# Kernel tuning notes

Hardware: AMD Instinct MI355X
Metric: run time of the kernel (lower is better)

## Reference

```python
import jax, jax.numpy as jnp
import numpy as np
from jax import lax

BETA = 0.95
THRESHOLD = 1.0
B, T, D_IN, D_OUT = 128, 512, 512, 512


def setup_inputs() -> dict:
    key = jax.random.key(0)
    k1, k2, k3 = jax.random.split(key, 3)
    x_seq = jax.random.normal(k1, (B, T, D_IN), dtype=jnp.float32)
    W = jax.random.normal(k2, (D_OUT, D_IN), dtype=jnp.float32) * (1.0 / np.sqrt(D_IN))
    b = jax.random.normal(k3, (D_OUT,), dtype=jnp.float32) * 0.01
    return {"x_seq": x_seq, "W": W, "b": b}


def reference(x_seq, W, b):
    # Batch the linear across all timesteps: [B,T,D_in] @ [D_out,D_in]^T -> [B,T,D_out]
    currents = jnp.einsum('bti,oi->bto', x_seq, W) + b

    def step(mem, cur):  # mem: [B, D_out], cur: [B, D_out]
        mem = BETA * mem + cur
        spk = (mem > THRESHOLD).astype(mem.dtype)
        return mem - spk * THRESHOLD, spk

    mem0 = jnp.zeros((x_seq.shape[0], W.shape[0]), dtype=x_seq.dtype)
    _, spikes_tbd = lax.scan(step, mem0, jnp.swapaxes(currents, 0, 1))  # [T,B,D]
    spikes = jnp.swapaxes(spikes_tbd, 0, 1)  # [B,T,D]
    return spikes, spikes.sum()
```

## Files before the change

### kernel.cpp

```cpp
#include <hip/hip_runtime.h>
#include <hip/hip_bf16.h>

#define M_TOT 65536
#define K_DIM 512
#define N_DIM 512
#define T_STEPS 512
#define BETA 0.95f

#define BM 128
#define BN 128
#define BK 64

typedef __attribute__((ext_vector_type(8))) short bf16x8;
typedef __attribute__((ext_vector_type(8))) unsigned short u16x8;
typedef __attribute__((ext_vector_type(4))) float f32x4;

#define X_ELEMS ((size_t)M_TOT * K_DIM)
#define W_ELEMS ((size_t)N_DIM * K_DIM)
#define WS_NEEDED ((X_ELEMS + W_ELEMS) * 2)

static __device__ __forceinline__ unsigned short f2bf(float f) {
    __hip_bfloat16 h = __float2bfloat16(f);
    return __builtin_bit_cast(unsigned short, h);
}

__global__ __launch_bounds__(256) void convert_bf16(
    const float* __restrict__ X, const float* __restrict__ W,
    unsigned short* __restrict__ Xb, unsigned short* __restrict__ Wb,
    float* __restrict__ sum_out)
{
    const size_t gid = (size_t)blockIdx.x * 256 + threadIdx.x;
    if (gid == 0) *sum_out = 0.0f;
    const size_t NXT = X_ELEMS / 8;
    if (gid < NXT) {
        const float4 v0 = *(const float4*)(X + gid * 8);
        const float4 v1 = *(const float4*)(X + gid * 8 + 4);
        u16x8 o;
        o[0] = f2bf(v0.x); o[1] = f2bf(v0.y); o[2] = f2bf(v0.z); o[3] = f2bf(v0.w);
        o[4] = f2bf(v1.x); o[5] = f2bf(v1.y); o[6] = f2bf(v1.z); o[7] = f2bf(v1.w);
        *(u16x8*)(Xb + gid * 8) = o;
    } else {
        const size_t g2 = gid - NXT;
        const float4 v0 = *(const float4*)(W + g2 * 8);
        const float4 v1 = *(const float4*)(W + g2 * 8 + 4);
        u16x8 o;
        o[0] = f2bf(v0.x); o[1] = f2bf(v0.y); o[2] = f2bf(v0.z); o[3] = f2bf(v0.w);
        o[4] = f2bf(v1.x); o[5] = f2bf(v1.y); o[6] = f2bf(v1.z); o[7] = f2bf(v1.w);
        *(u16x8*)(Wb + g2 * 8) = o;
    }
}

__global__ __launch_bounds__(256) void gemm_fast(
    const unsigned short* __restrict__ Xb,
    const unsigned short* __restrict__ Wb,
    const float* __restrict__ bias,
    float* __restrict__ C)
{
    __shared__ alignas(16) unsigned short Xs[BM][BK];
    __shared__ alignas(16) unsigned short Ws[BN][BK];

    const int lin  = blockIdx.x;
    const int swz  = (lin & 7) * 256 + (lin >> 3);
    const int mtile = swz >> 2;
    const int ntile = swz & 3;

    const int tid  = threadIdx.x;
    const int lane = tid & 63;
    const int wave = tid >> 6;
    const int wr = wave >> 1;
    const int wc = wave & 1;

    const int row0 = mtile * BM;
    const int col0 = ntile * BN;

    f32x4 acc[4][4] = {};

    const int srow = lane >> 3;
    const int scb  = (lane & 7) ^ (srow & 7);
    const unsigned short* xsrc[4];
    const unsigned short* wsrc[4];
    #pragma unroll
    for (int j = 0; j < 4; ++j) {
        const int ra = row0 + wave * 32 + j * 8 + srow;
        const int rb = col0 + wave * 32 + j * 8 + srow;
        xsrc[j] = Xb + (size_t)ra * K_DIM + scb * 8;
        wsrc[j] = Wb + (size_t)rb * K_DIM + scb * 8;
    }

    const int frow = lane & 15;
    const int cblk = lane >> 4;

    #pragma unroll
    for (int t = 0; t < 8; ++t) {
        if (t) __syncthreads();
        #pragma unroll
        for (int j = 0; j < 4; ++j) {
            __builtin_amdgcn_global_load_lds(
                (const __attribute__((address_space(1))) unsigned int*)(const void*)(xsrc[j] + t * BK),
                (__attribute__((address_space(3))) unsigned int*)(void*)(&Xs[wave * 32 + j * 8][0]),
                16, 0, 0);
            __builtin_amdgcn_global_load_lds(
                (const __attribute__((address_space(1))) unsigned int*)(const void*)(wsrc[j] + t * BK),
                (__attribute__((address_space(3))) unsigned int*)(void*)(&Ws[wave * 32 + j * 8][0]),
                16, 0, 0);
        }
        __syncthreads();

        #pragma unroll
        for (int kh = 0; kh < 2; ++kh) {
            bf16x8 afr[4], bfr[4];
            #pragma unroll
            for (int m = 0; m < 4; ++m) {
                int row = wr * 64 + m * 16 + frow;
                int c = (kh * 4 + cblk) ^ (row & 7);
                afr[m] = *(const bf16x8*)(&Xs[row][c * 8]);
            }
            #pragma unroll
            for (int n = 0; n < 4; ++n) {
                int row = wc * 64 + n * 16 + frow;
                int c = (kh * 4 + cblk) ^ (row & 7);
                bfr[n] = *(const bf16x8*)(&Ws[row][c * 8]);
            }
            #pragma unroll
            for (int m = 0; m < 4; ++m)
                #pragma unroll
                for (int n = 0; n < 4; ++n)
                    acc[m][n] = __builtin_amdgcn_mfma_f32_16x16x32_bf16(
                        afr[m], bfr[n], acc[m][n], 0, 0, 0);
        }
    }

    const int crow_base = (lane >> 4) * 4;
    const int ccol = lane & 15;
    #pragma unroll
    for (int n = 0; n < 4; ++n) {
        int col = col0 + wc * 64 + n * 16 + ccol;
        float bv = bias[col];
        #pragma unroll
        for (int m = 0; m < 4; ++m) {
            int rowb = row0 + wr * 64 + m * 16 + crow_base;
            #pragma unroll
            for (int r = 0; r < 4; ++r) {
                C[(size_t)(rowb + r) * N_DIM + col] = acc[m][n][r] + bv;
            }
        }
    }
}

static __device__ __forceinline__ void stage_tiles(
    unsigned short (*__restrict__ Xs)[BK], unsigned short (*__restrict__ Ws)[BK],
    const float4* xr, const float4* wv, int sr0, int skg)
{
    #pragma unroll
    for (int i = 0; i < 8; ++i) {
        int r   = sr0 + i * 16;
        int kgs = skg ^ ((r & 7) << 3);
        ushort4 xb, wb;
        xb.x = f2bf(xr[i].x); xb.y = f2bf(xr[i].y); xb.z = f2bf(xr[i].z); xb.w = f2bf(xr[i].w);
        wb.x = f2bf(wv[i].x); wb.y = f2bf(wv[i].y); wb.z = f2bf(wv[i].z); wb.w = f2bf(wv[i].w);
        *(ushort4*)(&Xs[r][kgs]) = xb;
        *(ushort4*)(&Ws[r][kgs]) = wb;
    }
}

__global__ __launch_bounds__(256, 2) void gemm_slow(
    const float* __restrict__ X, const float* __restrict__ W,
    const float* __restrict__ bias, float* __restrict__ C,
    float* __restrict__ sum_out)
{
    __shared__ unsigned short Xs[2][BM][BK];
    __shared__ unsigned short Ws[2][BN][BK];

    const int lin  = blockIdx.x;
    const int swz  = (lin & 7) * 256 + (lin >> 3);
    const int mtile = swz >> 2;
    const int ntile = swz & 3;

    const int tid  = threadIdx.x;
    const int lane = tid & 63;
    const int wave = tid >> 6;
    const int wr = wave >> 1;
    const int wc = wave & 1;

    if (lin == 0 && tid == 0) *sum_out = 0.0f;

    const int row0 = mtile * BM;
    const int col0 = ntile * BN;

    f32x4 acc[4][4] = {};

    const int sr0 = tid >> 4;
    const int skg = (tid & 15) << 2;
    const float* xbase = X + (size_t)row0 * K_DIM + skg;
    const float* wbase = W + (size_t)col0 * K_DIM + skg;

    float4 xr[8], wv[8];
    #pragma unroll
    for (int i = 0; i < 8; ++i) {
        int r = sr0 + i * 16;
        xr[i] = *(const float4*)(xbase + (size_t)r * K_DIM);
        wv[i] = *(const float4*)(wbase + (size_t)r * K_DIM);
    }
    stage_tiles(Xs[0], Ws[0], xr, wv, sr0, skg);

    const int frow = lane & 15;
    const int cblk = lane >> 4;

    for (int t = 0; t < 8; ++t) {
        __syncthreads();
        if (t < 7) {
            const int k0n = (t + 1) * BK;
            #pragma unroll
            for (int i = 0; i < 8; ++i) {
                int r = sr0 + i * 16;
                xr[i] = *(const float4*)(xbase + (size_t)r * K_DIM + k0n);
                wv[i] = *(const float4*)(wbase + (size_t)r * K_DIM + k0n);
            }
        }
        unsigned short (*Xb)[BK] = Xs[t & 1];
        unsigned short (*Wb)[BK] = Ws[t & 1];
        #pragma unroll
        for (int kh = 0; kh < 2; ++kh) {
            bf16x8 afr[4], bfr[4];
            #pragma unroll
            for (int m = 0; m < 4; ++m) {
                int row = wr * 64 + m * 16 + frow;
                int c = (kh * 4 + cblk) ^ (row & 7);
                afr[m] = *(const bf16x8*)(&Xb[row][c * 8]);
            }
            #pragma unroll
            for (int n = 0; n < 4; ++n) {
                int row = wc * 64 + n * 16 + frow;
                int c = (kh * 4 + cblk) ^ (row & 7);
                bfr[n] = *(const bf16x8*)(&Wb[row][c * 8]);
            }
            #pragma unroll
            for (int m = 0; m < 4; ++m)
                #pragma unroll
                for (int n = 0; n < 4; ++n)
                    acc[m][n] = __builtin_amdgcn_mfma_f32_16x16x32_bf16(
                        afr[m], bfr[n], acc[m][n], 0, 0, 0);
        }
        if (t < 7)
            stage_tiles(Xs[(t + 1) & 1], Ws[(t + 1) & 1], xr, wv, sr0, skg);
    }

    const int crow_base = (lane >> 4) * 4;
    const int ccol = lane & 15;
    #pragma unroll
    for (int n = 0; n < 4; ++n) {
        int col = col0 + wc * 64 + n * 16 + ccol;
        float bv = bias[col];
        #pragma unroll
        for (int m = 0; m < 4; ++m) {
            int rowb = row0 + wr * 64 + m * 16 + crow_base;
            #pragma unroll
            for (int r = 0; r < 4; ++r) {
                C[(size_t)(rowb + r) * N_DIM + col] = acc[m][n][r] + bv;
            }
        }
    }
}

__global__ __launch_bounds__(256) void lif_scan(
    float* __restrict__ C,
    float* __restrict__ sum_out)
{
    const int idx = blockIdx.x * 256 + threadIdx.x;
    float* p = C + (size_t)(idx >> 9) * (T_STEPS * N_DIM) + (idx & 511);

    float mem = 0.0f;
    int count = 0;
    float a[32], b[32];

    #pragma unroll
    for (int j = 0; j < 32; ++j)
        a[j] = p[(size_t)j * N_DIM];

    for (int t = 0; t < T_STEPS; t += 64) {
        #pragma unroll
        for (int j = 0; j < 32; ++j)
            b[j] = p[(size_t)(t + 32 + j) * N_DIM];
        #pragma unroll
        for (int j = 0; j < 32; ++j) {
            mem = BETA * mem + a[j];
            float spk = (mem > 1.0f) ? 1.0f : 0.0f;
            mem -= spk;
            __builtin_nontemporal_store(spk, p + (size_t)(t + j) * N_DIM);
            count += (int)spk;
        }
        if (t + 64 < T_STEPS) {
            #pragma unroll
            for (int j = 0; j < 32; ++j)
                a[j] = p[(size_t)(t + 64 + j) * N_DIM];
        }
        #pragma unroll
        for (int j = 0; j < 32; ++j) {
            mem = BETA * mem + b[j];
            float spk = (mem > 1.0f) ? 1.0f : 0.0f;
            mem -= spk;
            __builtin_nontemporal_store(spk, p + (size_t)(t + 32 + j) * N_DIM);
            count += (int)spk;
        }
    }

    #pragma unroll
    for (int off = 32; off > 0; off >>= 1)
        count += __shfl_down(count, off);
    __shared__ int wsum[4];
    if ((threadIdx.x & 63) == 0) wsum[threadIdx.x >> 6] = count;
    __syncthreads();
    if (threadIdx.x == 0) {
        int tot = wsum[0] + wsum[1] + wsum[2] + wsum[3];
        atomicAdd(sum_out, (float)tot);
    }
}

extern "C" void kernel_launch(void* const* d_in, const int* in_sizes, int n_in,
                              void* d_out, int out_size, void* d_ws, size_t ws_size,
                              hipStream_t stream) {
    const float* X    = (const float*)d_in[0];
    const float* W    = (const float*)d_in[1];
    const float* bias = (const float*)d_in[2];
    float* out = (float*)d_out;
    float* sum_slot = out + (size_t)M_TOT * N_DIM;

    if (ws_size >= WS_NEEDED) {
        unsigned short* Xb = (unsigned short*)d_ws;
        unsigned short* Wb = Xb + X_ELEMS;
        const int nconv = (int)((X_ELEMS / 8 + W_ELEMS / 8) / 256);
        convert_bf16<<<nconv, 256, 0, stream>>>(X, W, Xb, Wb, sum_slot);
        gemm_fast<<<(M_TOT / BM) * (N_DIM / BN), 256, 0, stream>>>(Xb, Wb, bias, out);
    } else {
        gemm_slow<<<(M_TOT / BM) * (N_DIM / BN), 256, 0, stream>>>(X, W, bias, out, sum_slot);
    }
    lif_scan<<<M_TOT / 256, 256, 0, stream>>>(out, sum_slot);
}
```

Baseline: 315.5 us.

## Store GEMM output as bf16 in workspace and double-buffer LDS loads

The GEMM now writes bias-added currents as bf16 into a workspace buffer instead of fp32 into the output. The scan reads these bf16 values and writes fp32 spikes to the output, which halves the intermediate write and read traffic. The fast GEMM also gains double-buffered global_load_lds prefetch, so the next K tile loads while the current one is computed. Rounding currents to bf16 can flip spikes near the threshold and change the recurrence, and the workspace requirement grows.

```diff
diff --git a/kernel.cpp b/kernel.cpp
--- a/kernel.cpp
+++ b/kernel.cpp
@@ -17,11 +17,14 @@
 
 #define X_ELEMS ((size_t)M_TOT * K_DIM)
 #define W_ELEMS ((size_t)N_DIM * K_DIM)
-#define WS_NEEDED ((X_ELEMS + W_ELEMS) * 2)
+#define WS_NEEDED ((X_ELEMS + W_ELEMS + X_ELEMS) * 2)
 
 static __device__ __forceinline__ unsigned short f2bf(float f) {
     __hip_bfloat16 h = __float2bfloat16(f);
     return __builtin_bit_cast(unsigned short, h);
+}
+static __device__ __forceinline__ float bf2f(unsigned short u) {
+    return __builtin_bit_cast(float, (unsigned int)u << 16);
 }
 
 __global__ __launch_bounds__(256) void convert_bf16(
@@ -54,10 +57,10 @@
     const unsigned short* __restrict__ Xb,
     const unsigned short* __restrict__ Wb,
     const float* __restrict__ bias,
-    float* __restrict__ C)
-{
-    __shared__ alignas(16) unsigned short Xs[BM][BK];
-    __shared__ alignas(16) unsigned short Ws[BN][BK];
+    unsigned short* __restrict__ Cb)
+{
+    __shared__ alignas(16) unsigned short Xs[2][BM][BK];
+    __shared__ alignas(16) unsigned short Ws[2][BN][BK];
 
     const int lin  = blockIdx.x;
     const int swz  = (lin & 7) * 256 + (lin >> 3);
@@ -91,20 +94,35 @@
     const int cblk = lane >> 4;
 
     #pragma unroll
+    for (int j = 0; j < 4; ++j) {
+        __builtin_amdgcn_global_load_lds(
+            (const __attribute__((address_space(1))) unsigned int*)(const void*)(xsrc[j]),
+            (__attribute__((address_space(3))) unsigned int*)(void*)(&Xs[0][wave * 32 + j * 8][0]),
+            16, 0, 0);
+        __builtin_amdgcn_global_load_lds(
+            (const __attribute__((address_space(1))) unsigned int*)(const void*)(wsrc[j]),
+            (__attribute__((address_space(3))) unsigned int*)(void*)(&Ws[0][wave * 32 + j * 8][0]),
+            16, 0, 0);
+    }
+
+    #pragma unroll
     for (int t = 0; t < 8; ++t) {
-        if (t) __syncthreads();
-        #pragma unroll
-        for (int j = 0; j < 4; ++j) {
-            __builtin_amdgcn_global_load_lds(
-                (const __attribute__((address_space(1))) unsigned int*)(const void*)(xsrc[j] + t * BK),
-                (__attribute__((address_space(3))) unsigned int*)(void*)(&Xs[wave * 32 + j * 8][0]),
-                16, 0, 0);
-            __builtin_amdgcn_global_load_lds(
-                (const __attribute__((address_space(1))) unsigned int*)(const void*)(wsrc[j] + t * BK),
-                (__attribute__((address_space(3))) unsigned int*)(void*)(&Ws[wave * 32 + j * 8][0]),
-                16, 0, 0);
-        }
+        const int cur = t & 1;
         __syncthreads();
+
+        if (t < 7) {
+            #pragma unroll
+            for (int j = 0; j < 4; ++j) {
+                __builtin_amdgcn_global_load_lds(
+                    (const __attribute__((address_space(1))) unsigned int*)(const void*)(xsrc[j] + (t + 1) * BK),
+                    (__attribute__((address_space(3))) unsigned int*)(void*)(&Xs[cur ^ 1][wave * 32 + j * 8][0]),
+                    16, 0, 0);
+                __builtin_amdgcn_global_load_lds(
+                    (const __attribute__((address_space(1))) unsigned int*)(const void*)(wsrc[j] + (t + 1) * BK),
+                    (__attribute__((address_space(3))) unsigned int*)(void*)(&Ws[cur ^ 1][wave * 32 + j * 8][0]),
+                    16, 0, 0);
+            }
+        }
 
         #pragma unroll
         for (int kh = 0; kh < 2; ++kh) {
@@ -113,13 +131,13 @@
             for (int m = 0; m < 4; ++m) {
                 int row = wr * 64 + m * 16 + frow;
                 int c = (kh * 4 + cblk) ^ (row & 7);
-                afr[m] = *(const bf16x8*)(&Xs[row][c * 8]);
+                afr[m] = *(const bf16x8*)(&Xs[cur][row][c * 8]);
             }
             #pragma unroll
             for (int n = 0; n < 4; ++n) {
                 int row = wc * 64 + n * 16 + frow;
                 int c = (kh * 4 + cblk) ^ (row & 7);
-                bfr[n] = *(const bf16x8*)(&Ws[row][c * 8]);
+                bfr[n] = *(const bf16x8*)(&Ws[cur][row][c * 8]);
             }
             #pragma unroll
             for (int m = 0; m < 4; ++m)
@@ -141,9 +159,66 @@
             int rowb = row0 + wr * 64 + m * 16 + crow_base;
             #pragma unroll
             for (int r = 0; r < 4; ++r) {
-                C[(size_t)(rowb + r) * N_DIM + col] = acc[m][n][r] + bv;
-            }
-        }
+                Cb[(size_t)(rowb + r) * N_DIM + col] = f2bf(acc[m][n][r] + bv);
+            }
+        }
+    }
+}
+
+__global__ __launch_bounds__(256) void lif_scan(
+    const unsigned short* __restrict__ Cb,
+    float* __restrict__ S,
+    float* __restrict__ sum_out)
+{
+    const int idx = blockIdx.x * 256 + threadIdx.x;
+    const size_t base = (size_t)(idx >> 9) * (T_STEPS * N_DIM) + (idx & 511);
+    const unsigned short* p = Cb + base;
+    float* q = S + base;
+
+    float mem = 0.0f;
+    int count = 0;
+    float a[32], b[32];
+
+    #pragma unroll
+    for (int j = 0; j < 32; ++j)
+        a[j] = bf2f(p[(size_t)j * N_DIM]);
+
+    for (int t = 0; t < T_STEPS; t += 64) {
+        #pragma unroll
+        for (int j = 0; j < 32; ++j)
+            b[j] = bf2f(p[(size_t)(t + 32 + j) * N_DIM]);
+        #pragma unroll
+        for (int j = 0; j < 32; ++j) {
+            mem = BETA * mem + a[j];
+            float spk = (mem > 1.0f) ? 1.0f : 0.0f;
+            mem -= spk;
+            __builtin_nontemporal_store(spk, q + (size_t)(t + j) * N_DIM);
+            count += (int)spk;
+        }
+        if (t + 64 < T_STEPS) {
+            #pragma unroll
+            for (int j = 0; j < 32; ++j)
+                a[j] = bf2f(p[(size_t)(t + 64 + j) * N_DIM]);
+        }
+        #pragma unroll
+        for (int j = 0; j < 32; ++j) {
+            mem = BETA * mem + b[j];
+            float spk = (mem > 1.0f) ? 1.0f : 0.0f;
+            mem -= spk;
+            __builtin_nontemporal_store(spk, q + (size_t)(t + 32 + j) * N_DIM);
+            count += (int)spk;
+        }
+    }
+
+    #pragma unroll
+    for (int off = 32; off > 0; off >>= 1)
+        count += __shfl_down(count, off);
+    __shared__ int wsum[4];
+    if ((threadIdx.x & 63) == 0) wsum[threadIdx.x >> 6] = count;
+    __syncthreads();
+    if (threadIdx.x == 0) {
+        int tot = wsum[0] + wsum[1] + wsum[2] + wsum[3];
+        atomicAdd(sum_out, (float)tot);
     }
 }
 
@@ -217,8 +292,8 @@
                 wv[i] = *(const float4*)(wbase + (size_t)r * K_DIM + k0n);
             }
         }
-        unsigned short (*Xb)[BK] = Xs[t & 1];
-        unsigned short (*Wb)[BK] = Ws[t & 1];
+        unsigned short (*Xbuf)[BK] = Xs[t & 1];
+        unsigned short (*Wbuf)[BK] = Ws[t & 1];
         #pragma unroll
         for (int kh = 0; kh < 2; ++kh) {
             bf16x8 afr[4], bfr[4];
@@ -226,13 +301,13 @@
             for (int m = 0; m < 4; ++m) {
                 int row = wr * 64 + m * 16 + frow;
                 int c = (kh * 4 + cblk) ^ (row & 7);
-                afr[m] = *(const bf16x8*)(&Xb[row][c * 8]);
+                afr[m] = *(const bf16x8*)(&Xbuf[row][c * 8]);
             }
             #pragma unroll
             for (int n = 0; n < 4; ++n) {
                 int row = wc * 64 + n * 16 + frow;
                 int c = (kh * 4 + cblk) ^ (row & 7);
-                bfr[n] = *(const bf16x8*)(&Wb[row][c * 8]);
+                bfr[n] = *(const bf16x8*)(&Wbuf[row][c * 8]);
             }
             #pragma unroll
             for (int m = 0; m < 4; ++m)
@@ -262,58 +337,33 @@
     }
 }
 
-__global__ __launch_bounds__(256) void lif_scan(
-    float* __restrict__ C,
-    float* __restrict__ sum_out)
+__global__ __launch_bounds__(256) void lif_scan_f32(
+    float* __restrict__ C, float* __restrict__ sum_out)
 {
     const int idx = blockIdx.x * 256 + threadIdx.x;
     float* p = C + (size_t)(idx >> 9) * (T_STEPS * N_DIM) + (idx & 511);
-
     float mem = 0.0f;
     int count = 0;
-    float a[32], b[32];
-
-    #pragma unroll
-    for (int j = 0; j < 32; ++j)
-        a[j] = p[(size_t)j * N_DIM];
-
-    for (int t = 0; t < T_STEPS; t += 64) {
-        #pragma unroll
-        for (int j = 0; j < 32; ++j)
-            b[j] = p[(size_t)(t + 32 + j) * N_DIM];
-        #pragma unroll
-        for (int j = 0; j < 32; ++j) {
-            mem = BETA * mem + a[j];
+    for (int t = 0; t < T_STEPS; t += 8) {
+        float cur[8];
+        #pragma unroll
+        for (int j = 0; j < 8; ++j) cur[j] = p[(size_t)(t + j) * N_DIM];
+        #pragma unroll
+        for (int j = 0; j < 8; ++j) {
+            mem = BETA * mem + cur[j];
             float spk = (mem > 1.0f) ? 1.0f : 0.0f;
             mem -= spk;
-            __builtin_nontemporal_store(spk, p + (size_t)(t + j) * N_DIM);
+            p[(size_t)(t + j) * N_DIM] = spk;
             count += (int)spk;
         }
-        if (t + 64 < T_STEPS) {
-            #pragma unroll
-            for (int j = 0; j < 32; ++j)
-                a[j] = p[(size_t)(t + 64 + j) * N_DIM];
-        }
-        #pragma unroll
-        for (int j = 0; j < 32; ++j) {
-            mem = BETA * mem + b[j];
-            float spk = (mem > 1.0f) ? 1.0f : 0.0f;
-            mem -= spk;
-            __builtin_nontemporal_store(spk, p + (size_t)(t + 32 + j) * N_DIM);
-            count += (int)spk;
-        }
-    }
-
-    #pragma unroll
-    for (int off = 32; off > 0; off >>= 1)
-        count += __shfl_down(count, off);
+    }
+    #pragma unroll
+    for (int off = 32; off > 0; off >>= 1) count += __shfl_down(count, off);
     __shared__ int wsum[4];
     if ((threadIdx.x & 63) == 0) wsum[threadIdx.x >> 6] = count;
     __syncthreads();
-    if (threadIdx.x == 0) {
-        int tot = wsum[0] + wsum[1] + wsum[2] + wsum[3];
-        atomicAdd(sum_out, (float)tot);
-    }
+    if (threadIdx.x == 0)
+        atomicAdd(sum_out, (float)(wsum[0] + wsum[1] + wsum[2] + wsum[3]));
 }
 
 extern "C" void kernel_launch(void* const* d_in, const int* in_sizes, int n_in,
@@ -328,11 +378,13 @@
     if (ws_size >= WS_NEEDED) {
         unsigned short* Xb = (unsigned short*)d_ws;
         unsigned short* Wb = Xb + X_ELEMS;
+        unsigned short* Cb = Wb + W_ELEMS;
         const int nconv = (int)((X_ELEMS / 8 + W_ELEMS / 8) / 256);
         convert_bf16<<<nconv, 256, 0, stream>>>(X, W, Xb, Wb, sum_slot);
-        gemm_fast<<<(M_TOT / BM) * (N_DIM / BN), 256, 0, stream>>>(Xb, Wb, bias, out);
+        gemm_fast<<<(M_TOT / BM) * (N_DIM / BN), 256, 0, stream>>>(Xb, Wb, bias, Cb);
+        lif_scan<<<M_TOT / 256, 256, 0, stream>>>(Cb, out, sum_slot);
     } else {
         gemm_slow<<<(M_TOT / BM) * (N_DIM / BN), 256, 0, stream>>>(X, W, bias, out, sum_slot);
-    }
-    lif_scan<<<M_TOT / 256, 256, 0, stream>>>(out, sum_slot);
-}
+        lif_scan_f32<<<M_TOT / 256, 256, 0, stream>>>(out, sum_slot);
+    }
+}
```

After: 317.2 us. No clear change (+0.5%).
